# Optimization experiments

Measured on AMD Instinct MI355X. Metric: run time of the kernel, lower is better.

## Reference

```python
import jax, jax.numpy as jnp
import numpy as np

V, E, H, OUT, T = 100000, 300, 512, 1, 2048


def setup_inputs() -> dict:
    key = jax.random.key(0)
    ks = jax.random.split(key, 15)
    s = 0.04  # ~1/sqrt(hidden) init scale
    return {
        "sentA": jax.random.randint(ks[0], (T,), 0, V),
        "sentB": jax.random.randint(ks[1], (T,), 0, V),
        "hidden": jnp.zeros((2, 2, H), jnp.float32),  # unused by forward, kept for signature fidelity
        "emb": jax.random.normal(ks[2], (V, E), jnp.float32) * 0.1,
        "w_ih": jax.random.normal(ks[3], (2, 4 * H, E), jnp.float32) * s,
        "w_hh": jax.random.normal(ks[4], (2, 4 * H, H), jnp.float32) * s,
        "b_ih": jax.random.normal(ks[5], (2, 4 * H), jnp.float32) * s,
        "b_hh": jax.random.normal(ks[6], (2, 4 * H), jnp.float32) * s,
        "bi_w": jax.random.uniform(ks[7], (1, 2), jnp.float32, -0.5, 0.5),
        "bi_b": jax.random.normal(ks[8], (1,), jnp.float32) * s,
        "blA": jax.random.uniform(ks[9], (H, H), jnp.float32, -0.1, 0.1),
        "blB": jax.random.uniform(ks[10], (H, H), jnp.float32, -0.1, 0.1),
        "bl_b": jax.random.normal(ks[11], (H,), jnp.float32) * s,
        "out_w": jax.random.uniform(ks[12], (OUT, H), jnp.float32, -0.1, 0.1),
        "out_b": jax.random.normal(ks[13], (OUT,), jnp.float32) * s,
    }


def _lstm_dir(x, w_ih, w_hh, b_ih, b_hh):
    # x: [T, E]; single-direction LSTM, returns final hidden state h_T [H]
    gx = x @ w_ih.T + (b_ih + b_hh)  # [T, 4H] input-gate preactivations, hoisted out of scan
    h_dim = w_hh.shape[1]

    def step(carry, g_t):
        h, c = carry
        g = g_t + h @ w_hh.T  # [4H]
        i, f, gg, o = jnp.split(g, 4, axis=-1)  # PyTorch gate order: i, f, g, o
        c = jax.nn.sigmoid(f) * c + jax.nn.sigmoid(i) * jnp.tanh(gg)
        h = jax.nn.sigmoid(o) * jnp.tanh(c)
        return (h, c), None

    init = (jnp.zeros((h_dim,), x.dtype), jnp.zeros((h_dim,), x.dtype))
    (h, _), _ = jax.lax.scan(step, init, gx)
    return h


def _encode(sent, emb, w_ih, w_hh, b_ih, b_hh, bi_w, bi_b):
    x = emb[sent]  # [T, E]
    h_fwd = _lstm_dir(x, w_ih[0], w_hh[0], b_ih[0], b_hh[0])
    h_bwd = _lstm_dir(x[::-1], w_ih[1], w_hh[1], b_ih[1], b_hh[1])
    hid = jnp.stack([h_fwd, h_bwd])  # [2, H]
    # bi_weight(hid.t()).t(): mixes the 2 directions per hidden unit -> [1, H]
    return bi_w @ hid + bi_b


def reference(sentA, sentB, hidden, emb, w_ih, w_hh, b_ih, b_hh,
              bi_w, bi_b, blA, blB, bl_b, out_w, out_b):
    hA = _encode(sentA, emb, w_ih, w_hh, b_ih, b_hh, bi_w, bi_b)  # [1, H]
    hB = _encode(sentB, emb, w_ih, w_hh, b_ih, b_hh, bi_w, bi_b)  # [1, H]
    # Double_Linear: A @ WA + B @ WB + bias
    biout = hA @ blA + hB @ blB + bl_b  # [1, H]
    out_l = jnp.tanh(biout) @ out_w.T + out_b  # [1, OUT]
    return jax.nn.sigmoid(out_l)
```

## Files before the change

kernel.cpp:

```cpp
#include <hip/hip_runtime.h>
#include <hip/hip_bf16.h>

#define T_LEN 2048
#define E_DIM 300
#define H_DIM 512
#define G_DIM 2048
#define NBLK  32
#define UPB   16
#define TAG_OFF 0x40000000u

#define WS_H   0
#define WS_X   16384
#define WS_GX  5242880

typedef float v2f __attribute__((ext_vector_type(2)));

__device__ __forceinline__ float sigmoid_fast(float x) {
    return 1.f / (1.f + __expf(-x));
}
__device__ __forceinline__ float tanh_fast(float x) {
    x = fminf(fmaxf(x, -15.f), 15.f);
    float e = __expf(-2.f * x);
    return (1.f - e) / (1.f + e);
}

__global__ void k_gather(const int* __restrict__ sentA, const int* __restrict__ sentB,
                         const float* __restrict__ emb, float* __restrict__ x) {
    const int s = blockIdx.y;
    const int* sent = s ? sentB : sentA;
    const int t0 = blockIdx.x * 16;
    for (int idx = threadIdx.x; idx < 16 * 300; idx += 256) {
        int r = idx / 300, e = idx - r * 300;
        int t = t0 + r;
        int row = sent[t];
        x[((size_t)(s * 2048 + t)) * 300 + e] = emb[(size_t)row * 300 + e];
    }
}

__global__ __launch_bounds__(256) void k_gemm(const float* __restrict__ x,
                                              const float* __restrict__ w_ih,
                                              const float* __restrict__ b_ih,
                                              const float* __restrict__ b_hh,
                                              __hip_bfloat16* __restrict__ gx) {
    __shared__ float xs[32 * 108];
    __shared__ float ws_[64 * 108];
    const int gi = blockIdx.x, ti = blockIdx.y, z = blockIdx.z;
    const int d = z >> 1, s = z & 1;
    const int t0 = ti * 32, g0 = gi * 64;
    const int tg = threadIdx.x & 15, tt = threadIdx.x >> 4;
    const float* wbase = w_ih + (size_t)d * G_DIM * E_DIM;

    float acc[2][4];
#pragma unroll
    for (int j = 0; j < 2; ++j)
#pragma unroll
        for (int i = 0; i < 4; ++i) acc[j][i] = 0.f;

    for (int e0 = 0; e0 < 300; e0 += 100) {
        for (int idx = threadIdx.x; idx < 32 * 25; idx += 256) {
            int r = idx / 25, c = idx - r * 25;
            float4 v = *(const float4*)(x + ((size_t)(s * 2048 + t0 + r)) * 300 + e0 + c * 4);
            *(float4*)&xs[r * 108 + c * 4] = v;
        }
        for (int idx = threadIdx.x; idx < 64 * 25; idx += 256) {
            int r = idx / 25, c = idx - r * 25;
            float4 v = *(const float4*)(wbase + (size_t)(g0 + r) * 300 + e0 + c * 4);
            *(float4*)&ws_[r * 108 + c * 4] = v;
        }
        __syncthreads();

        for (int c = 0; c < 25; ++c) {
            float4 xv[2], wv[4];
#pragma unroll
            for (int j = 0; j < 2; ++j) xv[j] = *(const float4*)&xs[(tt + 16 * j) * 108 + c * 4];
#pragma unroll
            for (int i = 0; i < 4; ++i) wv[i] = *(const float4*)&ws_[(tg + 16 * i) * 108 + c * 4];
#pragma unroll
            for (int j = 0; j < 2; ++j)
#pragma unroll
                for (int i = 0; i < 4; ++i)
                    acc[j][i] += xv[j].x * wv[i].x + xv[j].y * wv[i].y +
                                 xv[j].z * wv[i].z + xv[j].w * wv[i].w;
        }
        __syncthreads();
    }

#pragma unroll
    for (int i = 0; i < 4; ++i) {
        int g = g0 + tg + 16 * i;
        float bias = b_ih[d * G_DIM + g] + b_hh[d * G_DIM + g];
        int pos = ((g >> 4) & 31) * 64 + (g >> 9) * 16 + (g & 15);
#pragma unroll
        for (int j = 0; j < 2; ++j) {
            int t = t0 + tt + 16 * j;
            int tout = d ? (T_LEN - 1 - t) : t;
            float v = acc[j][i] + bias;
            gx[(((size_t)(d * 2 + s) * T_LEN + tout) << 11) + pos] = __float2bfloat16(v);
        }
    }
}

__global__ __launch_bounds__(256, 1) void k_rnn(const float* __restrict__ w_hh,
                                                const __hip_bfloat16* __restrict__ gx,
                                                unsigned long long* __restrict__ hb) {
    const int tid  = threadIdx.x;
    const int lane = tid & 63;
    const int w    = tid >> 6;
    const int sub  = tid & 3;
    const int q_g  = (tid >> 2) & 3;
    const int ul_g = tid >> 4;
    const int bid = blockIdx.x;
    const int d  = bid >> 6;
    const int s  = (bid >> 5) & 1;
    const int bb = bid & 31;

    v2f wreg2[8][8];
#pragma unroll
    for (int r2 = 0; r2 < 8; ++r2)
#pragma unroll
        for (int kb = 0; kb < 8; ++kb) {
            const float* wp = w_hh + ((size_t)d * G_DIM + w * 512 + bb * 16 + 2 * r2) * H_DIM
                            + kb * 64 + lane;
            v2f t2; t2.x = wp[0]; t2.y = wp[H_DIM];
            wreg2[r2][kb] = t2;
        }

    __shared__ float hlds[H_DIM];
    __shared__ float pacc[64 * 68];

    float c_state = 0.f;

    if ((lane & 15) == 0) {
        __hip_atomic_store(&hb[((size_t)(d * 2 + 0) * 2 + s) * H_DIM + bb * UPB + ul_g],
                           (unsigned long long)TAG_OFF << 32,
                           __ATOMIC_RELAXED, __HIP_MEMORY_SCOPE_AGENT);
    }

    const int i0 = w * 128 + lane;
    const int i1 = i0 + 64;

    for (int t = 0; t < T_LEN; ++t) {
        const int p  = t & 1;
        const int pn = p ^ 1;

        float gxv = (float)gx[(((size_t)(d * 2 + s) * T_LEN + t) << 11)
                              + bb * 64 + q_g * 16 + ul_g];

        unsigned long long* hbp = hb + ((size_t)(d * 2 + p) * 2 + s) * H_DIM;
        const unsigned int tag = TAG_OFF + (unsigned int)t;
        unsigned long long a0, a1, b0, b1;

#define LDH(X) __hip_atomic_load(&hbp[X], __ATOMIC_RELAXED, __HIP_MEMORY_SCOPE_AGENT)
        a0 = LDH(i0); a1 = LDH(i1);
        int guard = 0;
        for (;;) {
            b0 = LDH(i0); b1 = LDH(i1);
            bool okA = ((unsigned int)(a0 >> 32) == tag) & ((unsigned int)(a1 >> 32) == tag);
            if (__all(okA)) break;
            if (++guard > (1 << 20)) break;
            a0 = LDH(i0); a1 = LDH(i1);
            bool okB = ((unsigned int)(b0 >> 32) == tag) & ((unsigned int)(b1 >> 32) == tag);
            if (__all(okB)) { a0 = b0; a1 = b1; break; }
            if (++guard > (1 << 20)) break;
        }
#undef LDH

        hlds[i0] = __uint_as_float((unsigned int)a0);
        hlds[i1] = __uint_as_float((unsigned int)a1);
        __syncthreads();

        float hv[8];
#pragma unroll
        for (int kb = 0; kb < 8; ++kb)
            hv[kb] = hlds[kb * 64 + lane];

        v2f acc2[8];
#pragma unroll
        for (int r2 = 0; r2 < 8; ++r2) acc2[r2] = (v2f)(0.f);
#pragma unroll
        for (int kb = 0; kb < 8; ++kb) {
            float h0 = hv[kb];
            v2f h2; h2.x = h0; h2.y = h0;
#pragma unroll
            for (int r2 = 0; r2 < 8; ++r2)
                acc2[r2] += wreg2[r2][kb] * h2;
        }

#pragma unroll
        for (int r2 = 0; r2 < 8; ++r2) {
            pacc[((2 * r2 + 0) * 4 + w) * 68 + lane] = acc2[r2].x;
            pacc[((2 * r2 + 1) * 4 + w) * 68 + lane] = acc2[r2].y;
        }
        __syncthreads();

        const float4* pr = (const float4*)&pacc[(tid >> 2) * 68 + sub * 16];
        float4 sv = pr[0];
#pragma unroll
        for (int j2 = 1; j2 < 4; ++j2) {
            float4 q4 = pr[j2];
            sv.x += q4.x; sv.y += q4.y; sv.z += q4.z; sv.w += q4.w;
        }
        float v = (sv.x + sv.y) + (sv.z + sv.w);
        v += __shfl_xor(v, 1, 64);
        v += __shfl_xor(v, 2, 64);
        v += gxv;
        float act = (q_g == 2) ? tanh_fast(v) : sigmoid_fast(v);

        const int g0l = lane & ~15;
        float si = __shfl(act, g0l + 0,  64);
        float sf = __shfl(act, g0l + 4,  64);
        float tg = __shfl(act, g0l + 8,  64);
        float so = __shfl(act, g0l + 12, 64);
        if ((lane & 15) == 0) {
            c_state = sf * c_state + si * tg;
            float h_new = so * tanh_fast(c_state);
            unsigned long long pkt = ((unsigned long long)(TAG_OFF + (unsigned int)(t + 1)) << 32)
                                   | (unsigned long long)__float_as_uint(h_new);
            __hip_atomic_store(&hb[((size_t)(d * 2 + pn) * 2 + s) * H_DIM + bb * UPB + ul_g],
                               pkt, __ATOMIC_RELAXED, __HIP_MEMORY_SCOPE_AGENT);
        }
    }
}

__global__ __launch_bounds__(512) void k_head(const unsigned long long* __restrict__ hb,
                                              const float* __restrict__ bi_w,
                                              const float* __restrict__ bi_b,
                                              const float* __restrict__ blA,
                                              const float* __restrict__ blB,
                                              const float* __restrict__ bl_b,
                                              const float* __restrict__ out_w,
                                              const float* __restrict__ out_b,
                                              float* __restrict__ out) {
    __shared__ float enc[2][512];
    __shared__ float red[8];
    const int tid = threadIdx.x;
    const float bw0 = bi_w[0], bw1 = bi_w[1], bib = bi_b[0];
    {
        int u = tid;
        float hfA = __uint_as_float((unsigned int)hb[((0 * 2 + 0) * 2 + 0) * 512 + u]);
        float hbA = __uint_as_float((unsigned int)hb[((1 * 2 + 0) * 2 + 0) * 512 + u]);
        float hfB = __uint_as_float((unsigned int)hb[((0 * 2 + 0) * 2 + 1) * 512 + u]);
        float hbB = __uint_as_float((unsigned int)hb[((1 * 2 + 0) * 2 + 1) * 512 + u]);
        enc[0][u] = bw0 * hfA + bw1 * hbA + bib;
        enc[1][u] = bw0 * hfB + bw1 * hbB + bib;
    }
    __syncthreads();
    const int j = tid;
    float acc = bl_b[j];
#pragma unroll 4
    for (int u = 0; u < 512; ++u)
        acc += enc[0][u] * blA[u * 512 + j] + enc[1][u] * blB[u * 512 + j];
    float contrib = tanh_fast(acc) * out_w[j];
#pragma unroll
    for (int m = 1; m < 64; m <<= 1) contrib += __shfl_xor(contrib, m, 64);
    if ((tid & 63) == 0) red[tid >> 6] = contrib;
    __syncthreads();
    if (tid == 0) {
        float s = 0.f;
#pragma unroll
        for (int i = 0; i < 8; ++i) s += red[i];
        s += out_b[0];
        out[0] = sigmoid_fast(s);
    }
}

extern "C" void kernel_launch(void* const* d_in, const int* in_sizes, int n_in,
                              void* d_out, int out_size, void* d_ws, size_t ws_size,
                              hipStream_t stream) {
    const int*   sentA = (const int*)d_in[0];
    const int*   sentB = (const int*)d_in[1];
    const float* emb   = (const float*)d_in[3];
    const float* w_ih  = (const float*)d_in[4];
    const float* w_hh  = (const float*)d_in[5];
    const float* b_ih  = (const float*)d_in[6];
    const float* b_hh  = (const float*)d_in[7];
    const float* bi_w  = (const float*)d_in[8];
    const float* bi_b  = (const float*)d_in[9];
    const float* blA   = (const float*)d_in[10];
    const float* blB   = (const float*)d_in[11];
    const float* bl_b  = (const float*)d_in[12];
    const float* out_w = (const float*)d_in[13];
    const float* out_b = (const float*)d_in[14];
    float* out = (float*)d_out;

    char* ws = (char*)d_ws;
    unsigned long long* hbf = (unsigned long long*)(ws + WS_H);
    float*              x   = (float*)(ws + WS_X);
    __hip_bfloat16*     gx  = (__hip_bfloat16*)(ws + WS_GX);

    k_gather<<<dim3(128, 2), 256, 0, stream>>>(sentA, sentB, emb, x);
    k_gemm<<<dim3(32, 64, 4), 256, 0, stream>>>(x, w_ih, b_ih, b_hh, gx);
    k_rnn<<<dim3(128), 256, 0, stream>>>(w_hh, gx, hbf);
    k_head<<<dim3(1), 512, 0, stream>>>(hbf, bi_w, bi_b, blA, blB, bl_b, out_w, out_b, out);
}
```

Before: 4.423 ms.

## Make each wave own whole hidden units to remove block barriers in LSTM step

Repartitions the recurrent matvec so each wavefront owns four hidden units (all four gates) with K split across 16 lanes. Each wave now polls the full h vector itself into a private, swizzled, double-buffered LDS slice. This removes both __syncthreads and the cross-wave partial-sum LDS reduction per timestep. The cost is four times more polling loads per wave, since every wave reads all 512 h values, plus a 16-lane shuffle reduction.

```diff
diff --git a/kernel.cpp b/kernel.cpp
--- a/kernel.cpp
+++ b/kernel.cpp
@@ -106,117 +106,115 @@
     const int tid  = threadIdx.x;
     const int lane = tid & 63;
     const int w    = tid >> 6;
-    const int sub  = tid & 3;
-    const int q_g  = (tid >> 2) & 3;
-    const int ul_g = tid >> 4;
+    const int ul2  = lane >> 4;
+    const int ks   = lane & 15;
     const int bid = blockIdx.x;
     const int d  = bid >> 6;
     const int s  = (bid >> 5) & 1;
     const int bb = bid & 31;
-
-    v2f wreg2[8][8];
-#pragma unroll
-    for (int r2 = 0; r2 < 8; ++r2)
-#pragma unroll
-        for (int kb = 0; kb < 8; ++kb) {
-            const float* wp = w_hh + ((size_t)d * G_DIM + w * 512 + bb * 16 + 2 * r2) * H_DIM
-                            + kb * 64 + lane;
-            v2f t2; t2.x = wp[0]; t2.y = wp[H_DIM];
-            wreg2[r2][kb] = t2;
-        }
-
-    __shared__ float hlds[H_DIM];
-    __shared__ float pacc[64 * 68];
+    const int cs = d * 2 + s;
+    const int ul = w * 4 + ul2;
+    const int gu = bb * 16 + ul;
+
+    v2f wv2[4][16];
+#pragma unroll
+    for (int q = 0; q < 4; ++q) {
+        const float* wp = w_hh + ((size_t)d * G_DIM + q * 512 + gu) * H_DIM + ks * 32;
+#pragma unroll
+        for (int j = 0; j < 16; ++j)
+            wv2[q][j] = *(const v2f*)(wp + 2 * j);
+    }
+
+    __shared__ float hw[4][2][512];
 
     float c_state = 0.f;
 
-    if ((lane & 15) == 0) {
-        __hip_atomic_store(&hb[((size_t)(d * 2 + 0) * 2 + s) * H_DIM + bb * UPB + ul_g],
+    if (tid < 16) {
+        __hip_atomic_store(&hb[((size_t)(d * 2 + 0) * 2 + s) * H_DIM + bb * UPB + tid],
                            (unsigned long long)TAG_OFF << 32,
                            __ATOMIC_RELAXED, __HIP_MEMORY_SCOPE_AGENT);
     }
-
-    const int i0 = w * 128 + lane;
-    const int i1 = i0 + 64;
 
     for (int t = 0; t < T_LEN; ++t) {
         const int p  = t & 1;
         const int pn = p ^ 1;
 
-        float gxv = (float)gx[(((size_t)(d * 2 + s) * T_LEN + t) << 11)
-                              + bb * 64 + q_g * 16 + ul_g];
+        float gxq[4];
+        {
+            const __hip_bfloat16* gp = gx + (((size_t)cs * T_LEN + t) << 11) + bb * 64 + ul;
+#pragma unroll
+            for (int q = 0; q < 4; ++q) gxq[q] = (float)gp[q * 16];
+        }
 
         unsigned long long* hbp = hb + ((size_t)(d * 2 + p) * 2 + s) * H_DIM;
         const unsigned int tag = TAG_OFF + (unsigned int)t;
-        unsigned long long a0, a1, b0, b1;
-
-#define LDH(X) __hip_atomic_load(&hbp[X], __ATOMIC_RELAXED, __HIP_MEMORY_SCOPE_AGENT)
-        a0 = LDH(i0); a1 = LDH(i1);
+        unsigned long long a[8], b[8];
+
+#define LD8(A) _Pragma("unroll") for (int jj = 0; jj < 8; ++jj) \
+            A[jj] = __hip_atomic_load(&hbp[64 * jj + lane], __ATOMIC_RELAXED, __HIP_MEMORY_SCOPE_AGENT);
+#define OK8(A) (((unsigned int)(A[0] >> 32) == tag) & ((unsigned int)(A[1] >> 32) == tag) & \
+                ((unsigned int)(A[2] >> 32) == tag) & ((unsigned int)(A[3] >> 32) == tag) & \
+                ((unsigned int)(A[4] >> 32) == tag) & ((unsigned int)(A[5] >> 32) == tag) & \
+                ((unsigned int)(A[6] >> 32) == tag) & ((unsigned int)(A[7] >> 32) == tag))
+        LD8(a)
         int guard = 0;
         for (;;) {
-            b0 = LDH(i0); b1 = LDH(i1);
-            bool okA = ((unsigned int)(a0 >> 32) == tag) & ((unsigned int)(a1 >> 32) == tag);
-            if (__all(okA)) break;
+            LD8(b)
+            if (__all(OK8(a))) break;
             if (++guard > (1 << 20)) break;
-            a0 = LDH(i0); a1 = LDH(i1);
-            bool okB = ((unsigned int)(b0 >> 32) == tag) & ((unsigned int)(b1 >> 32) == tag);
-            if (__all(okB)) { a0 = b0; a1 = b1; break; }
+            LD8(a)
+            if (__all(OK8(b))) {
+#pragma unroll
+                for (int jj = 0; jj < 8; ++jj) a[jj] = b[jj];
+                break;
+            }
             if (++guard > (1 << 20)) break;
         }
-#undef LDH
-
-        hlds[i0] = __uint_as_float((unsigned int)a0);
-        hlds[i1] = __uint_as_float((unsigned int)a1);
-        __syncthreads();
-
-        float hv[8];
-#pragma unroll
-        for (int kb = 0; kb < 8; ++kb)
-            hv[kb] = hlds[kb * 64 + lane];
-
-        v2f acc2[8];
-#pragma unroll
-        for (int r2 = 0; r2 < 8; ++r2) acc2[r2] = (v2f)(0.f);
-#pragma unroll
-        for (int kb = 0; kb < 8; ++kb) {
-            float h0 = hv[kb];
-            v2f h2; h2.x = h0; h2.y = h0;
-#pragma unroll
-            for (int r2 = 0; r2 < 8; ++r2)
-                acc2[r2] += wreg2[r2][kb] * h2;
-        }
-
-#pragma unroll
-        for (int r2 = 0; r2 < 8; ++r2) {
-            pacc[((2 * r2 + 0) * 4 + w) * 68 + lane] = acc2[r2].x;
-            pacc[((2 * r2 + 1) * 4 + w) * 68 + lane] = acc2[r2].y;
-        }
-        __syncthreads();
-
-        const float4* pr = (const float4*)&pacc[(tid >> 2) * 68 + sub * 16];
-        float4 sv = pr[0];
-#pragma unroll
-        for (int j2 = 1; j2 < 4; ++j2) {
-            float4 q4 = pr[j2];
-            sv.x += q4.x; sv.y += q4.y; sv.z += q4.z; sv.w += q4.w;
-        }
-        float v = (sv.x + sv.y) + (sv.z + sv.w);
-        v += __shfl_xor(v, 1, 64);
-        v += __shfl_xor(v, 2, 64);
-        v += gxv;
-        float act = (q_g == 2) ? tanh_fast(v) : sigmoid_fast(v);
-
-        const int g0l = lane & ~15;
-        float si = __shfl(act, g0l + 0,  64);
-        float sf = __shfl(act, g0l + 4,  64);
-        float tg = __shfl(act, g0l + 8,  64);
-        float so = __shfl(act, g0l + 12, 64);
-        if ((lane & 15) == 0) {
-            c_state = sf * c_state + si * tg;
-            float h_new = so * tanh_fast(c_state);
-            unsigned long long pkt = ((unsigned long long)(TAG_OFF + (unsigned int)(t + 1)) << 32)
-                                   | (unsigned long long)__float_as_uint(h_new);
-            __hip_atomic_store(&hb[((size_t)(d * 2 + pn) * 2 + s) * H_DIM + bb * UPB + ul_g],
+#undef LD8
+#undef OK8
+
+        float* hwp = &hw[w][p][0];
+#pragma unroll
+        for (int jj = 0; jj < 8; ++jj) {
+            int e = 64 * jj + lane;
+            int L = e >> 2, sub = e & 3;
+            int Lp = L ^ ((L >> 3) & 7);
+            hwp[Lp * 4 + sub] = __uint_as_float((unsigned int)a[jj]);
+        }
+
+        v2f acc2[4];
+#pragma unroll
+        for (int q = 0; q < 4; ++q) acc2[q] = (v2f)(0.f);
+#pragma unroll
+        for (int jj = 0; jj < 8; ++jj) {
+            int Lp = (ks * 8 + jj) ^ (ks & 7);
+            float4 h4 = *(const float4*)&hwp[Lp * 4];
+            v2f h2a; h2a.x = h4.x; h2a.y = h4.y;
+            v2f h2b; h2b.x = h4.z; h2b.y = h4.w;
+#pragma unroll
+            for (int q = 0; q < 4; ++q)
+                acc2[q] += wv2[q][2 * jj] * h2a + wv2[q][2 * jj + 1] * h2b;
+        }
+
+        float vq[4];
+#pragma unroll
+        for (int q = 0; q < 4; ++q) vq[q] = acc2[q].x + acc2[q].y;
+#pragma unroll
+        for (int m = 1; m < 16; m <<= 1)
+#pragma unroll
+            for (int q = 0; q < 4; ++q) vq[q] += __shfl_xor(vq[q], m, 64);
+
+        float i_ = sigmoid_fast(vq[0] + gxq[0]);
+        float f_ = sigmoid_fast(vq[1] + gxq[1]);
+        float g_ = tanh_fast(vq[2] + gxq[2]);
+        float o_ = sigmoid_fast(vq[3] + gxq[3]);
+
+        c_state = f_ * c_state + i_ * g_;
+        float h_new = o_ * tanh_fast(c_state);
+        unsigned long long pkt = ((unsigned long long)(TAG_OFF + (unsigned int)(t + 1)) << 32)
+                               | (unsigned long long)__float_as_uint(h_new);
+        if (ks == 0) {
+            __hip_atomic_store(&hb[((size_t)(d * 2 + pn) * 2 + s) * H_DIM + gu],
                                pkt, __ATOMIC_RELAXED, __HIP_MEMORY_SCOPE_AGENT);
         }
     }
```

Measured after the change: 7.334 ms. +65.8%, slower.

## Use bf16 MFMA for input-gate GEMM and split head across blocks

Applied to the files above, without the earlier changes.

The input-projection GEMM now converts x and w_ih tiles to bf16 in shared memory and computes them with 16x16x32 bf16 MFMA instructions over the full padded K=320, replacing the scalar fp32 FMA loop. The head kernel is split into a 16-block kernel that computes partial Double_Linear outputs in parallel, plus a tiny reduction kernel, instead of one 512-thread block doing the whole 512x512 product. Rounding inputs to bf16 before the GEMM adds precision loss, and the head now costs an extra launch. The recurrent kernel, which probably dominates the time, is unchanged.

```diff
diff --git a/kernel.cpp b/kernel.cpp
--- a/kernel.cpp
+++ b/kernel.cpp
@@ -9,11 +9,14 @@
 #define UPB   16
 #define TAG_OFF 0x40000000u
 
-#define WS_H   0
-#define WS_X   16384
-#define WS_GX  5242880
+#define WS_H    0
+#define WS_X    16384
+#define WS_GX   5242880
+#define WS_OUT  38797312
 
 typedef float v2f __attribute__((ext_vector_type(2)));
+typedef __attribute__((ext_vector_type(8))) short bf16x8;
+typedef __attribute__((ext_vector_type(4))) float f32x4;
 
 __device__ __forceinline__ float sigmoid_fast(float x) {
     return 1.f / (1.f + __expf(-x));
@@ -22,6 +25,10 @@
     x = fminf(fmaxf(x, -15.f), 15.f);
     float e = __expf(-2.f * x);
     return (1.f - e) / (1.f + e);
+}
+__device__ __forceinline__ unsigned short bf16b(float f) {
+    __hip_bfloat16 h = __float2bfloat16(f);
+    unsigned short u; __builtin_memcpy(&u, &h, 2); return u;
 }
 
 __global__ void k_gather(const int* __restrict__ sentA, const int* __restrict__ sentB,
@@ -37,65 +44,63 @@
     }
 }
 
+#define KP 328
 __global__ __launch_bounds__(256) void k_gemm(const float* __restrict__ x,
                                               const float* __restrict__ w_ih,
                                               const float* __restrict__ b_ih,
                                               const float* __restrict__ b_hh,
                                               __hip_bfloat16* __restrict__ gx) {
-    __shared__ float xs[32 * 108];
-    __shared__ float ws_[64 * 108];
+    __shared__ unsigned short xs[32 * KP];
+    __shared__ unsigned short ws_[64 * KP];
     const int gi = blockIdx.x, ti = blockIdx.y, z = blockIdx.z;
     const int d = z >> 1, s = z & 1;
     const int t0 = ti * 32, g0 = gi * 64;
-    const int tg = threadIdx.x & 15, tt = threadIdx.x >> 4;
+    const int tid  = threadIdx.x;
+    const int lane = tid & 63, w = tid >> 6;
     const float* wbase = w_ih + (size_t)d * G_DIM * E_DIM;
 
-    float acc[2][4];
-#pragma unroll
-    for (int j = 0; j < 2; ++j)
-#pragma unroll
-        for (int i = 0; i < 4; ++i) acc[j][i] = 0.f;
-
-    for (int e0 = 0; e0 < 300; e0 += 100) {
-        for (int idx = threadIdx.x; idx < 32 * 25; idx += 256) {
-            int r = idx / 25, c = idx - r * 25;
-            float4 v = *(const float4*)(x + ((size_t)(s * 2048 + t0 + r)) * 300 + e0 + c * 4);
-            *(float4*)&xs[r * 108 + c * 4] = v;
-        }
-        for (int idx = threadIdx.x; idx < 64 * 25; idx += 256) {
-            int r = idx / 25, c = idx - r * 25;
-            float4 v = *(const float4*)(wbase + (size_t)(g0 + r) * 300 + e0 + c * 4);
-            *(float4*)&ws_[r * 108 + c * 4] = v;
-        }
-        __syncthreads();
-
-        for (int c = 0; c < 25; ++c) {
-            float4 xv[2], wv[4];
-#pragma unroll
-            for (int j = 0; j < 2; ++j) xv[j] = *(const float4*)&xs[(tt + 16 * j) * 108 + c * 4];
-#pragma unroll
-            for (int i = 0; i < 4; ++i) wv[i] = *(const float4*)&ws_[(tg + 16 * i) * 108 + c * 4];
-#pragma unroll
-            for (int j = 0; j < 2; ++j)
-#pragma unroll
-                for (int i = 0; i < 4; ++i)
-                    acc[j][i] += xv[j].x * wv[i].x + xv[j].y * wv[i].y +
-                                 xv[j].z * wv[i].z + xv[j].w * wv[i].w;
-        }
-        __syncthreads();
-    }
-
-#pragma unroll
-    for (int i = 0; i < 4; ++i) {
-        int g = g0 + tg + 16 * i;
+    for (int idx = tid; idx < 32 * 80; idx += 256) {
+        int r = idx / 80, c = idx - r * 80;
+        float4 v = {0.f, 0.f, 0.f, 0.f};
+        if (c < 75) v = *(const float4*)(x + ((size_t)(s * 2048 + t0 + r)) * 300 + c * 4);
+        ushort4 o; o.x = bf16b(v.x); o.y = bf16b(v.y); o.z = bf16b(v.z); o.w = bf16b(v.w);
+        *(ushort4*)&xs[r * KP + c * 4] = o;
+    }
+    for (int idx = tid; idx < 64 * 80; idx += 256) {
+        int r = idx / 80, c = idx - r * 80;
+        float4 v = {0.f, 0.f, 0.f, 0.f};
+        if (c < 75) v = *(const float4*)(wbase + (size_t)(g0 + r) * 300 + c * 4);
+        ushort4 o; o.x = bf16b(v.x); o.y = bf16b(v.y); o.z = bf16b(v.z); o.w = bf16b(v.w);
+        *(ushort4*)&ws_[r * KP + c * 4] = o;
+    }
+    __syncthreads();
+
+    const int mw = (w & 1) * 16, nb = (w >> 1) * 32;
+    const int fm = lane & 15;
+    const int fk = (lane >> 4) * 8;
+    f32x4 acc0 = {0.f, 0.f, 0.f, 0.f};
+    f32x4 acc1 = {0.f, 0.f, 0.f, 0.f};
+#pragma unroll
+    for (int e0 = 0; e0 < 320; e0 += 32) {
+        bf16x8 av  = *(const bf16x8*)&xs[(mw + fm) * KP + e0 + fk];
+        bf16x8 bv0 = *(const bf16x8*)&ws_[(nb + fm) * KP + e0 + fk];
+        bf16x8 bv1 = *(const bf16x8*)&ws_[(nb + 16 + fm) * KP + e0 + fk];
+        acc0 = __builtin_amdgcn_mfma_f32_16x16x32_bf16(av, bv0, acc0, 0, 0, 0);
+        acc1 = __builtin_amdgcn_mfma_f32_16x16x32_bf16(av, bv1, acc1, 0, 0, 0);
+    }
+
+    const int trowb = (lane >> 4) * 4;
+#pragma unroll
+    for (int nt = 0; nt < 2; ++nt) {
+        f32x4 a = nt ? acc1 : acc0;
+        int g = g0 + nb + nt * 16 + fm;
         float bias = b_ih[d * G_DIM + g] + b_hh[d * G_DIM + g];
         int pos = ((g >> 4) & 31) * 64 + (g >> 9) * 16 + (g & 15);
 #pragma unroll
-        for (int j = 0; j < 2; ++j) {
-            int t = t0 + tt + 16 * j;
+        for (int i = 0; i < 4; ++i) {
+            int t = t0 + mw + trowb + i;
             int tout = d ? (T_LEN - 1 - t) : t;
-            float v = acc[j][i] + bias;
-            gx[(((size_t)(d * 2 + s) * T_LEN + tout) << 11) + pos] = __float2bfloat16(v);
+            gx[(((size_t)z * T_LEN + tout) << 11) + pos] = __float2bfloat16(a[i] + bias);
         }
     }
 }
@@ -222,21 +227,22 @@
     }
 }
 
-__global__ __launch_bounds__(512) void k_head(const unsigned long long* __restrict__ hb,
-                                              const float* __restrict__ bi_w,
-                                              const float* __restrict__ bi_b,
-                                              const float* __restrict__ blA,
-                                              const float* __restrict__ blB,
-                                              const float* __restrict__ bl_b,
-                                              const float* __restrict__ out_w,
-                                              const float* __restrict__ out_b,
-                                              float* __restrict__ out) {
+__global__ __launch_bounds__(256) void k_head1(const unsigned long long* __restrict__ hb,
+                                               const float* __restrict__ bi_w,
+                                               const float* __restrict__ bi_b,
+                                               const float* __restrict__ blA,
+                                               const float* __restrict__ blB,
+                                               const float* __restrict__ bl_b,
+                                               const float* __restrict__ out_w,
+                                               float* __restrict__ partial) {
     __shared__ float enc[2][512];
-    __shared__ float red[8];
+    __shared__ float red[8][36];
     const int tid = threadIdx.x;
+    const int jl = tid & 31;
+    const int ur = tid >> 5;
+    const int j  = blockIdx.x * 32 + jl;
     const float bw0 = bi_w[0], bw1 = bi_w[1], bib = bi_b[0];
-    {
-        int u = tid;
+    for (int u = tid; u < 512; u += 256) {
         float hfA = __uint_as_float((unsigned int)hb[((0 * 2 + 0) * 2 + 0) * 512 + u]);
         float hbA = __uint_as_float((unsigned int)hb[((1 * 2 + 0) * 2 + 0) * 512 + u]);
         float hfB = __uint_as_float((unsigned int)hb[((0 * 2 + 0) * 2 + 1) * 512 + u]);
@@ -245,23 +251,34 @@
         enc[1][u] = bw0 * hfB + bw1 * hbB + bib;
     }
     __syncthreads();
-    const int j = tid;
-    float acc = bl_b[j];
-#pragma unroll 4
-    for (int u = 0; u < 512; ++u)
-        acc += enc[0][u] * blA[u * 512 + j] + enc[1][u] * blB[u * 512 + j];
-    float contrib = tanh_fast(acc) * out_w[j];
-#pragma unroll
-    for (int m = 1; m < 64; m <<= 1) contrib += __shfl_xor(contrib, m, 64);
-    if ((tid & 63) == 0) red[tid >> 6] = contrib;
+    float acc = 0.f;
+    const int u0 = ur * 64;
+#pragma unroll 8
+    for (int k = 0; k < 64; ++k) {
+        int u = u0 + k;
+        acc += enc[0][u] * blA[(size_t)u * 512 + j] + enc[1][u] * blB[(size_t)u * 512 + j];
+    }
+    red[ur][jl] = acc;
     __syncthreads();
-    if (tid == 0) {
-        float s = 0.f;
-#pragma unroll
-        for (int i = 0; i < 8; ++i) s += red[i];
-        s += out_b[0];
-        out[0] = sigmoid_fast(s);
-    }
+    if (tid < 32) {
+        float a = bl_b[j];
+#pragma unroll
+        for (int r = 0; r < 8; ++r) a += red[r][tid];
+        float c = tanh_fast(a) * out_w[j];
+#pragma unroll
+        for (int m = 1; m < 32; m <<= 1) c += __shfl_xor(c, m, 64);
+        if (tid == 0) partial[blockIdx.x] = c;
+    }
+}
+
+__global__ void k_head2(const float* __restrict__ partial,
+                        const float* __restrict__ out_b,
+                        float* __restrict__ out) {
+    const int l = threadIdx.x;
+    float v = (l < 16) ? partial[l] : 0.f;
+#pragma unroll
+    for (int m = 1; m < 16; m <<= 1) v += __shfl_xor(v, m, 64);
+    if (l == 0) out[0] = sigmoid_fast(v + out_b[0]);
 }
 
 extern "C" void kernel_launch(void* const* d_in, const int* in_sizes, int n_in,
@@ -287,9 +304,11 @@
     unsigned long long* hbf = (unsigned long long*)(ws + WS_H);
     float*              x   = (float*)(ws + WS_X);
     __hip_bfloat16*     gx  = (__hip_bfloat16*)(ws + WS_GX);
+    float*              par = (float*)(ws + WS_OUT);
 
     k_gather<<<dim3(128, 2), 256, 0, stream>>>(sentA, sentB, emb, x);
     k_gemm<<<dim3(32, 64, 4), 256, 0, stream>>>(x, w_ih, b_ih, b_hh, gx);
     k_rnn<<<dim3(128), 256, 0, stream>>>(w_hh, gx, hbf);
-    k_head<<<dim3(1), 512, 0, stream>>>(hbf, bi_w, bi_b, blA, blB, bl_b, out_w, out_b, out);
-}
+    k_head1<<<dim3(16), 256, 0, stream>>>(hbf, bi_w, bi_b, blA, blB, bl_b, out_w, par);
+    k_head2<<<dim3(1), 64, 0, stream>>>(par, out_b, out);
+}
```

Measured after the change: 4.246 ms. -4.0%, faster.
